# Performance work log

Hardware: AMD Instinct MI355X
Metric: run time of the kernel (lower is better)

Reference implementation:

```python
import jax, jax.numpy as jnp
import numpy as np

B, N, K, D, H = 16384, 10, 5, 512, 2
HD = D // H  # 256
IMG = 512.0


def setup_inputs() -> dict:
    key = jax.random.key(0)
    ks = jax.random.split(key, 18)
    w = lambda k, shape: (jax.random.normal(k, shape) * 0.02).astype(jnp.float32)
    boxes = jax.random.uniform(ks[0], (B, N, 4), minval=0.0, maxval=IMG, dtype=jnp.float32)
    return {
        'boxes': boxes,
        'w_in': w(ks[1], (D, K * 4)), 'b_in': jnp.zeros((D,), jnp.float32),
        'wqkv': w(ks[2], (3 * D, D)), 'bqkv': jnp.zeros((3 * D,), jnp.float32),
        'wo': w(ks[3], (D, D)), 'bo': jnp.zeros((D,), jnp.float32),
        'ln1_w': jnp.ones((D,), jnp.float32), 'ln1_b': jnp.zeros((D,), jnp.float32),
        'w1': w(ks[4], (D, D)), 'b1': jnp.zeros((D,), jnp.float32),
        'w2': w(ks[5], (D, D)), 'b2': jnp.zeros((D,), jnp.float32),
        'ln2_w': jnp.ones((D,), jnp.float32), 'ln2_b': jnp.zeros((D,), jnp.float32),
        'lnf_w': jnp.ones((D,), jnp.float32), 'lnf_b': jnp.zeros((D,), jnp.float32),
    }


def _ln(x, w, b, eps=1e-5):
    mu = jnp.mean(x, -1, keepdims=True)
    var = jnp.mean((x - mu) ** 2, -1, keepdims=True)
    return (x - mu) * jax.lax.rsqrt(var + eps) * w + b


def _relationships(boxes):
    # boxes: [B, N, 4] -> rel: [B, N, K*4]
    cx = (boxes[..., 0] + boxes[..., 2]) * 0.5 / IMG
    cy = (boxes[..., 1] + boxes[..., 3]) * 0.5 / IMG
    bw = jnp.abs(boxes[..., 2] - boxes[..., 0]) / IMG
    bh = jnp.abs(boxes[..., 3] - boxes[..., 1]) / IMG
    feats = jnp.stack([cx, cy, bw, bh], -1)  # [B, N, 4]
    dx = cx[:, :, None] - cx[:, None, :]
    dy = cy[:, :, None] - cy[:, None, :]
    dists = dx * dx + dy * dy  # [B, N, N]
    dists = jnp.where(jnp.eye(N, dtype=bool), jnp.inf, dists)
    _, idx = jax.lax.top_k(-dists, K)  # K smallest, ascending -> [B, N, K]
    nbr = jnp.take_along_axis(jnp.broadcast_to(feats[:, None], (B, N, N, 4)), idx[:, :, :, None], axis=2)  # [B, N, K, 4]
    return (nbr - feats[:, :, None, :]).reshape(B, N, K * 4)


def reference(boxes, w_in, b_in, wqkv, bqkv, wo, bo, ln1_w, ln1_b, w1, b1, w2, b2, ln2_w, ln2_b, lnf_w, lnf_b):
    rel = _relationships(boxes)                      # [B, N, 20]
    x = rel @ w_in.T + b_in                          # [B, N, D]
    # --- self attention (post-norm TransformerEncoderLayer, eval mode: no dropout) ---
    qkv = x @ wqkv.T + bqkv
    q, k, v = jnp.split(qkv, 3, axis=-1)
    split_heads = lambda t: t.reshape(B, N, H, HD).transpose(0, 2, 1, 3)
    q, k, v = split_heads(q), split_heads(k), split_heads(v)
    scores = jnp.einsum('bhqd,bhkd->bhqk', q, k) / jnp.sqrt(jnp.float32(HD))
    att = jax.nn.softmax(scores, axis=-1)
    o = jnp.einsum('bhqk,bhkd->bhqd', att, v).transpose(0, 2, 1, 3).reshape(B, N, D)
    x = _ln(x + o @ wo.T + bo, ln1_w, ln1_b)
    # --- feed forward ---
    ff = jax.nn.gelu(x @ w1.T + b1, approximate=False) @ w2.T + b2
    x = _ln(x + ff, ln2_w, ln2_b)
    return _ln(x, lnf_w, lnf_b)
```

## Files before the change

### kernel.cpp

```cpp
#include <hip/hip_runtime.h>
#include <hip/hip_bf16.h>
#include <math.h>

#define B_   16384
#define NT   10
#define KNN  5
#define D_   512
#define MTOT (B_*NT)

typedef __bf16 bf;
typedef __bf16 bfrag8 __attribute__((ext_vector_type(8)));
typedef float  floatx4 __attribute__((ext_vector_type(4)));

__device__ __forceinline__ float tof(bf x) { return (float)x; }
__device__ __forceinline__ bf    tob(float x) { return (bf)x; }

#define GLD_LDS(g, l) __builtin_amdgcn_global_load_lds( \
    (const __attribute__((address_space(1))) void*)(g), \
    (__attribute__((address_space(3))) void*)(l), 16, 0, 0)

__global__ void prep_folds(const float* __restrict__ wqkv, const float* __restrict__ bqkv,
                           const float* __restrict__ wo,   const float* __restrict__ bo,
                           bf* __restrict__ At, bf* __restrict__ Ct,
                           float* __restrict__ wconst, float* __restrict__ uvec)
{
    int gid = blockIdx.x, tid = threadIdx.x;
    if (gid < 4096) {
        int idx = gid * 256 + tid;
        int mat = idx >> 18;
        int rem = idx & 262143;
        int row = rem >> 9, col = rem & 511;
        float acc = 0.f;
        if (mat < 2) {
            int h = mat;
            const float* wq = wqkv + (size_t)(h * 256) * 512;
            const float* wk = wqkv + (size_t)(512 + h * 256) * 512;
            for (int c = 0; c < 256; ++c)
                acc += wq[c * 512 + col] * wk[c * 512 + row];
            At[(size_t)h * 262144 + row * 512 + col] = tob(acc * 0.0625f);
        } else {
            int h = mat - 2;
            const float* wv = wqkv + (size_t)(1024 + h * 256) * 512;
            for (int e = 0; e < 256; ++e)
                acc += wv[e * 512 + col] * wo[row * 512 + h * 256 + e];
            Ct[(size_t)h * 262144 + row * 512 + col] = tob(acc);
        }
    } else {
        for (int d = tid; d < 512; d += 256) {
            float acc = bo[d];
            for (int e = 0; e < 512; ++e)
                acc += bqkv[1024 + e] * wo[d * 512 + e];
            wconst[d] = acc;
            for (int h = 0; h < 2; ++h) {
                float u = 0.f;
                for (int c = 0; c < 256; ++c)
                    u += wqkv[(size_t)(512 + h * 256 + c) * 512 + d] * bqkv[h * 256 + c];
                uvec[h * 512 + d] = u * 0.0625f;
            }
        }
    }
}

__global__ void cvt_w(const float* __restrict__ src, bf* __restrict__ dst)
{
    int i = blockIdx.x * 256 + threadIdx.x;
    float4 v = *(const float4*)(src + (size_t)i * 4);
    bf4_store: ;
    bf o[4] = { tob(v.x), tob(v.y), tob(v.z), tob(v.w) };
    *(unsigned long long*)(dst + (size_t)i * 4) = *(unsigned long long*)o;
}

__global__ void rel_kernel(const float* __restrict__ boxes, float* __restrict__ rel)
{
#pragma clang fp contract(off)
    int gid = blockIdx.x * blockDim.x + threadIdx.x;
    if (gid >= MTOT) return;
    int b = gid / NT, n = gid % NT;
    const float* bx = boxes + (size_t)b * NT * 4;
    float cx[NT], cy[NT], bw[NT], bh[NT];
#pragma unroll
    for (int j = 0; j < NT; ++j) {
        float x0 = bx[j * 4 + 0], y0 = bx[j * 4 + 1];
        float x1 = bx[j * 4 + 2], y1 = bx[j * 4 + 3];
        cx[j] = ((x0 + x1) * 0.5f) * (1.f / 512.f);
        cy[j] = ((y0 + y1) * 0.5f) * (1.f / 512.f);
        bw[j] = fabsf(x1 - x0) * (1.f / 512.f);
        bh[j] = fabsf(y1 - y0) * (1.f / 512.f);
    }
    float dist[NT];
#pragma unroll
    for (int j = 0; j < NT; ++j) {
        float dx = cx[n] - cx[j], dy = cy[n] - cy[j];
        float dxx = dx * dx, dyy = dy * dy;
        dist[j] = (j == n) ? __builtin_inff() : (dxx + dyy);
    }
    float ocx = cx[n], ocy = cy[n], obw = bw[n], obh = bh[n];
#pragma unroll
    for (int k = 0; k < KNN; ++k) {
        int best = 0; float bd = __builtin_inff();
#pragma unroll
        for (int j = 0; j < NT; ++j)
            if (dist[j] < bd) { bd = dist[j]; best = j; }
        float fx = 0, fy = 0, fw = 0, fh = 0;
#pragma unroll
        for (int j = 0; j < NT; ++j)
            if (j == best) { fx = cx[j]; fy = cy[j]; fw = bw[j]; fh = bh[j]; dist[j] = __builtin_inff(); }
        size_t o = (size_t)gid * 20 + k * 4;
        rel[o + 0] = fx - ocx;
        rel[o + 1] = fy - ocy;
        rel[o + 2] = fw - obw;
        rel[o + 3] = fh - obh;
    }
}

__global__ void gemm_in(const float* __restrict__ rel, const float* __restrict__ w_in,
                        const float* __restrict__ b_in, bf* __restrict__ x0)
{
    __shared__ float relS[128][20];
    int tid = threadIdx.x;
    size_t tok0 = (size_t)blockIdx.x * 128;
    for (int i = tid; i < 128 * 20; i += 256)
        relS[i / 20][i % 20] = rel[tok0 * 20 + i];
    float w0[20], w1r[20];
#pragma unroll
    for (int j = 0; j < 20; ++j) {
        w0[j]  = w_in[tid * 20 + j];
        w1r[j] = w_in[(tid + 256) * 20 + j];
    }
    float bias0 = b_in[tid], bias1 = b_in[tid + 256];
    __syncthreads();
    for (int tk = 0; tk < 128; ++tk) {
        float a0 = bias0, a1 = bias1;
#pragma unroll
        for (int j = 0; j < 20; ++j) {
            float r = relS[tk][j];
            a0 += r * w0[j];
            a1 += r * w1r[j];
        }
        x0[(tok0 + tk) * 512 + tid]       = tob(a0);
        x0[(tok0 + tk) * 512 + tid + 256] = tob(a1);
    }
}

template <int EPI>
__launch_bounds__(256)
__global__ void gemm512(const bf* __restrict__ A, const bf* __restrict__ Bt,
                        bf* __restrict__ out, const float* __restrict__ biasf)
{
    __shared__ bf As[128 * 64];
    __shared__ bf Bs[128 * 64];
    int tid = threadIdx.x;
    int w = tid >> 6, l = tid & 63;
    int lq = l >> 4, lr = l & 15;
    int m0 = blockIdx.y * 128;
    int n0 = blockIdx.x * 128;
    int wm = (w & 1) * 64, wn = (w >> 1) * 64;
    floatx4 acc[4][4] = {};

    for (int kt = 0; kt < 8; ++kt) {
        int kb = kt * 64;
        __syncthreads();
#pragma unroll
        for (int i = 0; i < 4; ++i) {
            int chunk = i * 256 + tid;
            int mm = chunk & 127, kc = chunk >> 7;
            GLD_LDS(A  + (size_t)(m0 + mm) * 512 + kb + kc * 8, As + (i * 256 + w * 64) * 8);
            GLD_LDS(Bt + (size_t)(n0 + mm) * 512 + kb + kc * 8, Bs + (i * 256 + w * 64) * 8);
        }
        __syncthreads();
#pragma unroll
        for (int s = 0; s < 2; ++s) {
            bfrag8 af[4], bfv[4];
#pragma unroll
            for (int i = 0; i < 4; ++i)
                af[i] = *(const bfrag8*)(As + (size_t)((s * 4 + lq) * 128 + wm + i * 16 + lr) * 8);
#pragma unroll
            for (int j = 0; j < 4; ++j)
                bfv[j] = *(const bfrag8*)(Bs + (size_t)((s * 4 + lq) * 128 + wn + j * 16 + lr) * 8);
#pragma unroll
            for (int i = 0; i < 4; ++i)
#pragma unroll
                for (int j = 0; j < 4; ++j)
                    acc[i][j] = __builtin_amdgcn_mfma_f32_16x16x32_bf16(af[i], bfv[j], acc[i][j], 0, 0, 0);
        }
    }
#pragma unroll
    for (int i = 0; i < 4; ++i)
#pragma unroll
        for (int j = 0; j < 4; ++j) {
            int col = n0 + wn + j * 16 + lr;
#pragma unroll
            for (int r = 0; r < 4; ++r) {
                int row = m0 + wm + i * 16 + lq * 4 + r;
                float v = acc[i][j][r];
                if (EPI == 1) { v += biasf[col]; v = 0.5f * v * (1.f + erff(v * 0.70710678118654752f)); }
                if (EPI == 2) v += biasf[col];
                if (EPI == 3) v += tof(out[(size_t)row * 512 + col]);
                out[(size_t)row * 512 + col] = tob(v);
            }
        }
}

__global__ void scores_kernel(const bf* __restrict__ t, const bf* __restrict__ x0,
                              const float* __restrict__ uvec_h, float* __restrict__ att)
{
    int tid = threadIdx.x;
    int w = tid >> 6, l = tid & 63;
    int lq = l >> 4, lr = l & 15;
    size_t b = (size_t)blockIdx.x * 4 + w;
    const bf* trow = t  + (b * NT + lr) * 512;
    const bf* xrow = x0 + (b * NT + lr) * 512;
    floatx4 acc = {0.f, 0.f, 0.f, 0.f};
    float xu = 0.f;
#pragma unroll
    for (int kk = 0; kk < 16; ++kk) {
        bfrag8 a  = *(const bfrag8*)(trow + kk * 32 + lq * 8);
        bfrag8 bb = *(const bfrag8*)(xrow + kk * 32 + lq * 8);
        acc = __builtin_amdgcn_mfma_f32_16x16x32_bf16(a, bb, acc, 0, 0, 0);
#pragma unroll
        for (int jj = 0; jj < 8; ++jj)
            xu += (float)bb[jj] * uvec_h[kk * 32 + lq * 8 + jj];
    }
    xu += __shfl_xor(xu, 16);
    xu += __shfl_xor(xu, 32);
    bool jvalid = (lr < NT);
    float* ab = att + b * 100;
#pragma unroll
    for (int r = 0; r < 4; ++r) {
        float v = jvalid ? (acc[r] + xu) : -__builtin_inff();
        float m = v;
        m = fmaxf(m, __shfl_xor(m, 1)); m = fmaxf(m, __shfl_xor(m, 2));
        m = fmaxf(m, __shfl_xor(m, 4)); m = fmaxf(m, __shfl_xor(m, 8));
        float e = jvalid ? __expf(v - m) : 0.f;
        float s = e;
        s += __shfl_xor(s, 1); s += __shfl_xor(s, 2);
        s += __shfl_xor(s, 4); s += __shfl_xor(s, 8);
        float a = e / s;
        int i = lq * 4 + r;
        if (jvalid && i < NT) ab[i * 10 + lr] = a;
    }
}

__global__ void zmix(const float* __restrict__ att, const bf* __restrict__ x0, bf* __restrict__ z)
{
    __shared__ float xs[NT][512];
    __shared__ float as[100];
    size_t b = blockIdx.x;
    int tid = threadIdx.x;
    const bf* xb = x0 + b * NT * 512;
    for (int i = tid; i < NT * 512; i += 256) xs[i >> 9][i & 511] = tof(xb[i]);
    for (int i = tid; i < 100; i += 256) as[i] = att[b * 100 + i];
    __syncthreads();
    bf* zb = z + b * NT * 512;
    for (int o = tid; o < NT * 512; o += 256) {
        int i = o >> 9, d = o & 511;
        float a = 0.f;
#pragma unroll
        for (int j = 0; j < NT; ++j) a += as[i * 10 + j] * xs[j][d];
        zb[o] = tob(a);
    }
}

__global__ void ln_kernel(const bf* __restrict__ xin, const bf* __restrict__ yin,
                          const float* __restrict__ w, const float* __restrict__ bias,
                          bf* __restrict__ xout)
{
    int tid = threadIdx.x;
    int wv = tid >> 6, l = tid & 63;
    size_t tok = (size_t)blockIdx.x * 4 + wv;
    bfrag8 xv = *(const bfrag8*)(xin + tok * 512 + l * 8);
    bfrag8 yv = *(const bfrag8*)(yin + tok * 512 + l * 8);
    float v[8]; float s = 0.f;
#pragma unroll
    for (int i = 0; i < 8; ++i) { v[i] = (float)xv[i] + (float)yv[i]; s += v[i]; }
#pragma unroll
    for (int m = 1; m < 64; m <<= 1) s += __shfl_xor(s, m);
    float mu = s * (1.f / 512.f);
    float vs = 0.f;
#pragma unroll
    for (int i = 0; i < 8; ++i) { float d = v[i] - mu; vs += d * d; }
#pragma unroll
    for (int m = 1; m < 64; m <<= 1) vs += __shfl_xor(vs, m);
    float r = rsqrtf(vs * (1.f / 512.f) + 1e-5f);
    bfrag8 ov;
#pragma unroll
    for (int i = 0; i < 8; ++i) {
        int d = l * 8 + i;
        ov[i] = tob((v[i] - mu) * r * w[d] + bias[d]);
    }
    *(bfrag8*)(xout + tok * 512 + l * 8) = ov;
}

__global__ void final_kernel(const bf* __restrict__ x1, const bf* __restrict__ ff2,
                             const float* __restrict__ w2, const float* __restrict__ b2,
                             const float* __restrict__ wf, const float* __restrict__ bfi,
                             float* __restrict__ out)
{
    int tid = threadIdx.x;
    int wv = tid >> 6, l = tid & 63;
    size_t tok = (size_t)blockIdx.x * 4 + wv;
    bfrag8 xv = *(const bfrag8*)(x1 + tok * 512 + l * 8);
    bfrag8 yv = *(const bfrag8*)(ff2 + tok * 512 + l * 8);
    float v[8]; float s = 0.f;
#pragma unroll
    for (int i = 0; i < 8; ++i) { v[i] = (float)xv[i] + (float)yv[i]; s += v[i]; }
#pragma unroll
    for (int m = 1; m < 64; m <<= 1) s += __shfl_xor(s, m);
    float mu = s * (1.f / 512.f);
    float vs = 0.f;
#pragma unroll
    for (int i = 0; i < 8; ++i) { float d = v[i] - mu; vs += d * d; }
#pragma unroll
    for (int m = 1; m < 64; m <<= 1) vs += __shfl_xor(vs, m);
    float r = rsqrtf(vs * (1.f / 512.f) + 1e-5f);
    float u[8]; float s2 = 0.f;
#pragma unroll
    for (int i = 0; i < 8; ++i) {
        int d = l * 8 + i;
        u[i] = (v[i] - mu) * r * w2[d] + b2[d];
        s2 += u[i];
    }
#pragma unroll
    for (int m = 1; m < 64; m <<= 1) s2 += __shfl_xor(s2, m);
    float mu2 = s2 * (1.f / 512.f);
    float vs2 = 0.f;
#pragma unroll
    for (int i = 0; i < 8; ++i) { float d = u[i] - mu2; vs2 += d * d; }
#pragma unroll
    for (int m = 1; m < 64; m <<= 1) vs2 += __shfl_xor(vs2, m);
    float r2 = rsqrtf(vs2 * (1.f / 512.f) + 1e-5f);
    float4 o0, o1;
    float* op = (float*)&o0;
#pragma unroll
    for (int i = 0; i < 4; ++i) op[i] = (u[i] - mu2) * r2 * wf[l * 8 + i] + bfi[l * 8 + i];
    op = (float*)&o1;
#pragma unroll
    for (int i = 0; i < 4; ++i) op[i] = (u[4 + i] - mu2) * r2 * wf[l * 8 + 4 + i] + bfi[l * 8 + 4 + i];
    *(float4*)(out + tok * 512 + l * 8) = o0;
    *(float4*)(out + tok * 512 + l * 8 + 4) = o1;
}

extern "C" void kernel_launch(void* const* d_in, const int* in_sizes, int n_in,
                              void* d_out, int out_size, void* d_ws, size_t ws_size,
                              hipStream_t stream)
{
    const float* boxes = (const float*)d_in[0];
    const float* w_in  = (const float*)d_in[1];
    const float* b_in  = (const float*)d_in[2];
    const float* wqkv  = (const float*)d_in[3];
    const float* bqkv  = (const float*)d_in[4];
    const float* wo    = (const float*)d_in[5];
    const float* bo    = (const float*)d_in[6];
    const float* ln1w  = (const float*)d_in[7];
    const float* ln1b  = (const float*)d_in[8];
    const float* w1    = (const float*)d_in[9];
    const float* b1    = (const float*)d_in[10];
    const float* w2    = (const float*)d_in[11];
    const float* b2    = (const float*)d_in[12];
    const float* ln2w  = (const float*)d_in[13];
    const float* ln2b  = (const float*)d_in[14];
    const float* lnfw  = (const float*)d_in[15];
    const float* lnfb  = (const float*)d_in[16];
    float* out = (float*)d_out;

    char* ws = (char*)d_ws;
    bf*    At     = (bf*)(ws + 0);
    bf*    Ct     = (bf*)(ws + 1048576);
    bf*    W1b    = (bf*)(ws + 2097152);
    bf*    W2b    = (bf*)(ws + 2621440);
    float* wconst = (float*)(ws + 3145728);
    float* uvec   = (float*)(ws + 3147776);
    float* att    = (float*)(ws + 3151872);
    bf*    x0     = (bf*)(ws + 16259072);
    bf*    t      = (bf*)(ws + 184047616);
    bf*    y      = (bf*)(ws + 351836160);
    float* rel    = (float*)(ws + 184047616);

    dim3 gblk(256);
    dim3 ggemm(4, MTOT / 128);

    prep_folds<<<4097, gblk, 0, stream>>>(wqkv, bqkv, wo, bo, At, Ct, wconst, uvec);
    cvt_w<<<256, gblk, 0, stream>>>(w1, W1b);
    cvt_w<<<256, gblk, 0, stream>>>(w2, W2b);
    rel_kernel<<<(MTOT + 255) / 256, gblk, 0, stream>>>(boxes, rel);
    gemm_in<<<MTOT / 128, gblk, 0, stream>>>(rel, w_in, b_in, x0);

    gemm512<0><<<ggemm, gblk, 0, stream>>>(x0, At, t, nullptr);
    scores_kernel<<<B_ / 4, gblk, 0, stream>>>(t, x0, uvec, att);
    gemm512<0><<<ggemm, gblk, 0, stream>>>(x0, At + 262144, t, nullptr);
    scores_kernel<<<B_ / 4, gblk, 0, stream>>>(t, x0, uvec + 512, att + (size_t)B_ * 100);
    zmix<<<B_, gblk, 0, stream>>>(att, x0, t);
    gemm512<2><<<ggemm, gblk, 0, stream>>>(t, Ct, y, wconst);
    zmix<<<B_, gblk, 0, stream>>>(att + (size_t)B_ * 100, x0, t);
    gemm512<3><<<ggemm, gblk, 0, stream>>>(t, Ct + 262144, y, nullptr);
    ln_kernel<<<MTOT / 4, gblk, 0, stream>>>(x0, y, ln1w, ln1b, x0);
    gemm512<1><<<ggemm, gblk, 0, stream>>>(x0, W1b, t, b1);
    gemm512<2><<<ggemm, gblk, 0, stream>>>(t, W2b, y, b2);
    final_kernel<<<MTOT / 4, gblk, 0, stream>>>(x0, y, ln2w, ln2b, lnfw, lnfb, out);
}
```

Before: 2.578 ms.

## Fuse whole encoder layer into one persistent per-tile kernel with LDS-resident activations

Replaces the chain of separate kernels (input projection, per-head folded QK GEMMs, scores, zmix, output GEMMs, layernorms, FFN GEMMs, final LN) with a single kernel. Each block processes 80 tokens (8 batches of 10), keeping activations in swizzled LDS buffers and streaming weight fragments directly from global memory into MFMA operands with register double-buffering. This removes the large global round-trips of intermediate activations and the many kernel launches. In exchange, each block rereads every weight matrix, and the large LDS footprint and register use limit occupancy.

```diff
diff --git a/kernel.cpp b/kernel.cpp
--- a/kernel.cpp
+++ b/kernel.cpp
@@ -15,9 +15,12 @@
 __device__ __forceinline__ float tof(bf x) { return (float)x; }
 __device__ __forceinline__ bf    tob(float x) { return (bf)x; }
 
-#define GLD_LDS(g, l) __builtin_amdgcn_global_load_lds( \
-    (const __attribute__((address_space(1))) void*)(g), \
-    (__attribute__((address_space(3))) void*)(l), 16, 0, 0)
+__device__ __forceinline__ void sw_st16(bf* lds, int row, int col, bf v) {
+    *(bf*)((char*)lds + row * 1024 + ((col * 2) ^ ((row & 7) << 4))) = v;
+}
+__device__ __forceinline__ bf sw_ld16(const bf* lds, int row, int col) {
+    return *(const bf*)((const char*)lds + row * 1024 + ((col * 2) ^ ((row & 7) << 4)));
+}
 
 __global__ void prep_folds(const float* __restrict__ wqkv, const float* __restrict__ bqkv,
                            const float* __restrict__ wo,   const float* __restrict__ bo,
@@ -65,7 +68,6 @@
 {
     int i = blockIdx.x * 256 + threadIdx.x;
     float4 v = *(const float4*)(src + (size_t)i * 4);
-    bf4_store: ;
     bf o[4] = { tob(v.x), tob(v.y), tob(v.z), tob(v.w) };
     *(unsigned long long*)(dst + (size_t)i * 4) = *(unsigned long long*)o;
 }
@@ -113,231 +115,362 @@
     }
 }
 
-__global__ void gemm_in(const float* __restrict__ rel, const float* __restrict__ w_in,
-                        const float* __restrict__ b_in, bf* __restrict__ x0)
-{
-    __shared__ float relS[128][20];
-    int tid = threadIdx.x;
-    size_t tok0 = (size_t)blockIdx.x * 128;
-    for (int i = tid; i < 128 * 20; i += 256)
-        relS[i / 20][i % 20] = rel[tok0 * 20 + i];
-    float w0[20], w1r[20];
-#pragma unroll
-    for (int j = 0; j < 20; ++j) {
-        w0[j]  = w_in[tid * 20 + j];
-        w1r[j] = w_in[(tid + 256) * 20 + j];
-    }
-    float bias0 = b_in[tid], bias1 = b_in[tid + 256];
-    __syncthreads();
-    for (int tk = 0; tk < 128; ++tk) {
-        float a0 = bias0, a1 = bias1;
-#pragma unroll
-        for (int j = 0; j < 20; ++j) {
-            float r = relS[tk][j];
-            a0 += r * w0[j];
-            a1 += r * w1r[j];
-        }
-        x0[(tok0 + tk) * 512 + tid]       = tob(a0);
-        x0[(tok0 + tk) * 512 + tid + 256] = tob(a1);
-    }
-}
-
-template <int EPI>
-__launch_bounds__(256)
-__global__ void gemm512(const bf* __restrict__ A, const bf* __restrict__ Bt,
-                        bf* __restrict__ out, const float* __restrict__ biasf)
-{
-    __shared__ bf As[128 * 64];
-    __shared__ bf Bs[128 * 64];
-    int tid = threadIdx.x;
-    int w = tid >> 6, l = tid & 63;
-    int lq = l >> 4, lr = l & 15;
-    int m0 = blockIdx.y * 128;
-    int n0 = blockIdx.x * 128;
-    int wm = (w & 1) * 64, wn = (w >> 1) * 64;
-    floatx4 acc[4][4] = {};
-
-    for (int kt = 0; kt < 8; ++kt) {
-        int kb = kt * 64;
-        __syncthreads();
-#pragma unroll
-        for (int i = 0; i < 4; ++i) {
-            int chunk = i * 256 + tid;
-            int mm = chunk & 127, kc = chunk >> 7;
-            GLD_LDS(A  + (size_t)(m0 + mm) * 512 + kb + kc * 8, As + (i * 256 + w * 64) * 8);
-            GLD_LDS(Bt + (size_t)(n0 + mm) * 512 + kb + kc * 8, Bs + (i * 256 + w * 64) * 8);
-        }
-        __syncthreads();
-#pragma unroll
-        for (int s = 0; s < 2; ++s) {
-            bfrag8 af[4], bfv[4];
-#pragma unroll
-            for (int i = 0; i < 4; ++i)
-                af[i] = *(const bfrag8*)(As + (size_t)((s * 4 + lq) * 128 + wm + i * 16 + lr) * 8);
+__device__ __forceinline__ void gemm_ph(const bf* INlds, const bf* __restrict__ W,
+                                        floatx4 (&acc)[5][4], int w, int lq, int lr,
+                                        const int (&rb0)[5], const int (&sw0)[5])
+{
+    const bf* Wb = W + (size_t)(w * 64 + lr) * 512 + lq * 8;
+    bfrag8 bv[4], bn[4];
+#pragma unroll
+    for (int j = 0; j < 4; ++j) bv[j] = *(const bfrag8*)(Wb + (size_t)j * 8192);
+    for (int ks = 0; ks < 16; ++ks) {
+        if (ks < 15) {
 #pragma unroll
             for (int j = 0; j < 4; ++j)
-                bfv[j] = *(const bfrag8*)(Bs + (size_t)((s * 4 + lq) * 128 + wn + j * 16 + lr) * 8);
-#pragma unroll
-            for (int i = 0; i < 4; ++i)
-#pragma unroll
-                for (int j = 0; j < 4; ++j)
-                    acc[i][j] = __builtin_amdgcn_mfma_f32_16x16x32_bf16(af[i], bfv[j], acc[i][j], 0, 0, 0);
-        }
-    }
-#pragma unroll
-    for (int i = 0; i < 4; ++i)
-#pragma unroll
-        for (int j = 0; j < 4; ++j) {
-            int col = n0 + wn + j * 16 + lr;
-#pragma unroll
-            for (int r = 0; r < 4; ++r) {
-                int row = m0 + wm + i * 16 + lq * 4 + r;
-                float v = acc[i][j][r];
-                if (EPI == 1) { v += biasf[col]; v = 0.5f * v * (1.f + erff(v * 0.70710678118654752f)); }
-                if (EPI == 2) v += biasf[col];
-                if (EPI == 3) v += tof(out[(size_t)row * 512 + col]);
-                out[(size_t)row * 512 + col] = tob(v);
-            }
-        }
-}
-
-__global__ void scores_kernel(const bf* __restrict__ t, const bf* __restrict__ x0,
-                              const float* __restrict__ uvec_h, float* __restrict__ att)
-{
-    int tid = threadIdx.x;
-    int w = tid >> 6, l = tid & 63;
-    int lq = l >> 4, lr = l & 15;
-    size_t b = (size_t)blockIdx.x * 4 + w;
-    const bf* trow = t  + (b * NT + lr) * 512;
-    const bf* xrow = x0 + (b * NT + lr) * 512;
-    floatx4 acc = {0.f, 0.f, 0.f, 0.f};
+                bn[j] = *(const bfrag8*)(Wb + (size_t)j * 8192 + (ks + 1) * 32);
+        }
+        int cb = ks * 64 + lq * 16;
+        bfrag8 af[5];
+#pragma unroll
+        for (int i = 0; i < 5; ++i)
+            af[i] = *(const bfrag8*)((const char*)INlds + (rb0[i] + (cb ^ sw0[i])));
+#pragma unroll
+        for (int i = 0; i < 5; ++i)
+#pragma unroll
+            for (int j = 0; j < 4; ++j)
+                acc[i][j] = __builtin_amdgcn_mfma_f32_16x16x32_bf16(af[i], bv[j], acc[i][j], 0, 0, 0);
+#pragma unroll
+        for (int j = 0; j < 4; ++j) bv[j] = bn[j];
+    }
+}
+
+__device__ __forceinline__ void scores_z(const bf* Xs, bf* Ts, const float* __restrict__ uvec_h,
+                                         int w, int l, int lq, int lr)
+{
+    int rb = w * 10;
+    int arow = rb + (lr < 10 ? lr : 0);
+    int abase = arow * 1024, asw = (arow & 7) << 4;
+    floatx4 sacc = {0.f, 0.f, 0.f, 0.f};
     float xu = 0.f;
 #pragma unroll
     for (int kk = 0; kk < 16; ++kk) {
-        bfrag8 a  = *(const bfrag8*)(trow + kk * 32 + lq * 8);
-        bfrag8 bb = *(const bfrag8*)(xrow + kk * 32 + lq * 8);
-        acc = __builtin_amdgcn_mfma_f32_16x16x32_bf16(a, bb, acc, 0, 0, 0);
+        int cb = kk * 64 + lq * 16;
+        bfrag8 a  = *(const bfrag8*)((const char*)Ts + abase + (cb ^ asw));
+        bfrag8 bb = *(const bfrag8*)((const char*)Xs + abase + (cb ^ asw));
+        sacc = __builtin_amdgcn_mfma_f32_16x16x32_bf16(a, bb, sacc, 0, 0, 0);
 #pragma unroll
         for (int jj = 0; jj < 8; ++jj)
             xu += (float)bb[jj] * uvec_h[kk * 32 + lq * 8 + jj];
     }
     xu += __shfl_xor(xu, 16);
     xu += __shfl_xor(xu, 32);
-    bool jvalid = (lr < NT);
-    float* ab = att + b * 100;
+    bool jv = (lr < 10);
+    float a_r[4];
 #pragma unroll
     for (int r = 0; r < 4; ++r) {
-        float v = jvalid ? (acc[r] + xu) : -__builtin_inff();
+        float v = jv ? (sacc[r] + xu) : -__builtin_inff();
         float m = v;
         m = fmaxf(m, __shfl_xor(m, 1)); m = fmaxf(m, __shfl_xor(m, 2));
         m = fmaxf(m, __shfl_xor(m, 4)); m = fmaxf(m, __shfl_xor(m, 8));
-        float e = jvalid ? __expf(v - m) : 0.f;
+        float e = jv ? __expf(v - m) : 0.f;
         float s = e;
         s += __shfl_xor(s, 1); s += __shfl_xor(s, 2);
         s += __shfl_xor(s, 4); s += __shfl_xor(s, 8);
-        float a = e / s;
-        int i = lq * 4 + r;
-        if (jvalid && i < NT) ab[i * 10 + lr] = a;
-    }
-}
-
-__global__ void zmix(const float* __restrict__ att, const bf* __restrict__ x0, bf* __restrict__ z)
-{
-    __shared__ float xs[NT][512];
-    __shared__ float as[100];
-    size_t b = blockIdx.x;
+        a_r[r] = e / s;
+    }
+    bfrag8 xj[10];
+#pragma unroll
+    for (int j = 0; j < 10; ++j) {
+        int row = rb + j;
+        xj[j] = *(const bfrag8*)((const char*)Xs + row * 1024 + ((l * 16) ^ ((row & 7) << 4)));
+    }
+#pragma unroll
+    for (int i = 0; i < 10; ++i) {
+        float zz[8] = {0, 0, 0, 0, 0, 0, 0, 0};
+#pragma unroll
+        for (int j = 0; j < 10; ++j) {
+            float aij = __shfl(a_r[i & 3], ((i >> 2) << 4) + j);
+#pragma unroll
+            for (int q = 0; q < 8; ++q) zz[q] += aij * (float)xj[j][q];
+        }
+        bfrag8 zv;
+#pragma unroll
+        for (int q = 0; q < 8; ++q) zv[q] = tob(zz[q]);
+        int row = rb + i;
+        *(bfrag8*)((char*)Ts + row * 1024 + ((l * 16) ^ ((row & 7) << 4))) = zv;
+    }
+}
+
+__global__ __launch_bounds__(512, 2)
+void fused(const float* __restrict__ rel, const float* __restrict__ w_in,
+           const float* __restrict__ b_in,
+           const bf* __restrict__ At, const bf* __restrict__ Ct,
+           const float* __restrict__ uvec, const float* __restrict__ wconst,
+           const bf* __restrict__ W1b, const float* __restrict__ b1,
+           const bf* __restrict__ W2b, const float* __restrict__ b2,
+           const float* __restrict__ l1w, const float* __restrict__ l1b,
+           const float* __restrict__ l2w, const float* __restrict__ l2b,
+           const float* __restrict__ lfw, const float* __restrict__ lfb,
+           float* __restrict__ out)
+{
+    __shared__ __align__(16) bf Xs[40960];
+    __shared__ __align__(16) bf Ts[40960];
     int tid = threadIdx.x;
-    const bf* xb = x0 + b * NT * 512;
-    for (int i = tid; i < NT * 512; i += 256) xs[i >> 9][i & 511] = tof(xb[i]);
-    for (int i = tid; i < 100; i += 256) as[i] = att[b * 100 + i];
+    int w = tid >> 6, l = tid & 63, lq = l >> 4, lr = l & 15;
+    size_t tok0 = (size_t)blockIdx.x * 80;
+
+    {
+        float* relS = (float*)Ts;
+        for (int i = tid; i < 1600; i += 512) relS[i] = rel[tok0 * 20 + i];
+    }
     __syncthreads();
-    bf* zb = z + b * NT * 512;
-    for (int o = tid; o < NT * 512; o += 256) {
-        int i = o >> 9, d = o & 511;
-        float a = 0.f;
-#pragma unroll
-        for (int j = 0; j < NT; ++j) a += as[i * 10 + j] * xs[j][d];
-        zb[o] = tob(a);
-    }
-}
-
-__global__ void ln_kernel(const bf* __restrict__ xin, const bf* __restrict__ yin,
-                          const float* __restrict__ w, const float* __restrict__ bias,
-                          bf* __restrict__ xout)
-{
-    int tid = threadIdx.x;
-    int wv = tid >> 6, l = tid & 63;
-    size_t tok = (size_t)blockIdx.x * 4 + wv;
-    bfrag8 xv = *(const bfrag8*)(xin + tok * 512 + l * 8);
-    bfrag8 yv = *(const bfrag8*)(yin + tok * 512 + l * 8);
-    float v[8]; float s = 0.f;
-#pragma unroll
-    for (int i = 0; i < 8; ++i) { v[i] = (float)xv[i] + (float)yv[i]; s += v[i]; }
-#pragma unroll
-    for (int m = 1; m < 64; m <<= 1) s += __shfl_xor(s, m);
-    float mu = s * (1.f / 512.f);
-    float vs = 0.f;
-#pragma unroll
-    for (int i = 0; i < 8; ++i) { float d = v[i] - mu; vs += d * d; }
-#pragma unroll
-    for (int m = 1; m < 64; m <<= 1) vs += __shfl_xor(vs, m);
-    float r = rsqrtf(vs * (1.f / 512.f) + 1e-5f);
-    bfrag8 ov;
-#pragma unroll
-    for (int i = 0; i < 8; ++i) {
-        int d = l * 8 + i;
-        ov[i] = tob((v[i] - mu) * r * w[d] + bias[d]);
-    }
-    *(bfrag8*)(xout + tok * 512 + l * 8) = ov;
-}
-
-__global__ void final_kernel(const bf* __restrict__ x1, const bf* __restrict__ ff2,
-                             const float* __restrict__ w2, const float* __restrict__ b2,
-                             const float* __restrict__ wf, const float* __restrict__ bfi,
-                             float* __restrict__ out)
-{
-    int tid = threadIdx.x;
-    int wv = tid >> 6, l = tid & 63;
-    size_t tok = (size_t)blockIdx.x * 4 + wv;
-    bfrag8 xv = *(const bfrag8*)(x1 + tok * 512 + l * 8);
-    bfrag8 yv = *(const bfrag8*)(ff2 + tok * 512 + l * 8);
-    float v[8]; float s = 0.f;
-#pragma unroll
-    for (int i = 0; i < 8; ++i) { v[i] = (float)xv[i] + (float)yv[i]; s += v[i]; }
-#pragma unroll
-    for (int m = 1; m < 64; m <<= 1) s += __shfl_xor(s, m);
-    float mu = s * (1.f / 512.f);
-    float vs = 0.f;
-#pragma unroll
-    for (int i = 0; i < 8; ++i) { float d = v[i] - mu; vs += d * d; }
-#pragma unroll
-    for (int m = 1; m < 64; m <<= 1) vs += __shfl_xor(vs, m);
-    float r = rsqrtf(vs * (1.f / 512.f) + 1e-5f);
-    float u[8]; float s2 = 0.f;
-#pragma unroll
-    for (int i = 0; i < 8; ++i) {
-        int d = l * 8 + i;
-        u[i] = (v[i] - mu) * r * w2[d] + b2[d];
-        s2 += u[i];
-    }
-#pragma unroll
-    for (int m = 1; m < 64; m <<= 1) s2 += __shfl_xor(s2, m);
-    float mu2 = s2 * (1.f / 512.f);
-    float vs2 = 0.f;
-#pragma unroll
-    for (int i = 0; i < 8; ++i) { float d = u[i] - mu2; vs2 += d * d; }
-#pragma unroll
-    for (int m = 1; m < 64; m <<= 1) vs2 += __shfl_xor(vs2, m);
-    float r2 = rsqrtf(vs2 * (1.f / 512.f) + 1e-5f);
-    float4 o0, o1;
-    float* op = (float*)&o0;
-#pragma unroll
-    for (int i = 0; i < 4; ++i) op[i] = (u[i] - mu2) * r2 * wf[l * 8 + i] + bfi[l * 8 + i];
-    op = (float*)&o1;
-#pragma unroll
-    for (int i = 0; i < 4; ++i) op[i] = (u[4 + i] - mu2) * r2 * wf[l * 8 + 4 + i] + bfi[l * 8 + 4 + i];
-    *(float4*)(out + tok * 512 + l * 8) = o0;
-    *(float4*)(out + tok * 512 + l * 8 + 4) = o1;
+    {
+        const float* relS = (const float*)Ts;
+        float wreg[20];
+#pragma unroll
+        for (int k = 0; k < 20; ++k) wreg[k] = w_in[tid * 20 + k];
+        float bias = b_in[tid];
+        for (int r = 0; r < 80; ++r) {
+            float a = bias;
+#pragma unroll
+            for (int k = 0; k < 20; ++k) a += relS[r * 20 + k] * wreg[k];
+            sw_st16(Xs, r, tid, tob(a));
+        }
+    }
+    __syncthreads();
+
+    floatx4 acc[5][4];
+    floatx4 accY[5][4];
+    float   mus[5][4];
+    int rb0[5], sw0[5];
+#pragma unroll
+    for (int i = 0; i < 5; ++i) { int row = i * 16 + lr; rb0[i] = row * 1024; sw0[i] = (row & 7) << 4; }
+
+    for (int h = 0; h < 2; ++h) {
+#pragma unroll
+        for (int i = 0; i < 5; ++i)
+#pragma unroll
+            for (int j = 0; j < 4; ++j) acc[i][j] = (floatx4){0.f, 0.f, 0.f, 0.f};
+        gemm_ph(Xs, At + (size_t)h * 262144, acc, w, lq, lr, rb0, sw0);
+#pragma unroll
+        for (int i = 0; i < 5; ++i)
+#pragma unroll
+            for (int j = 0; j < 4; ++j) {
+                int col = w * 64 + j * 16 + lr;
+#pragma unroll
+                for (int r = 0; r < 4; ++r)
+                    sw_st16(Ts, i * 16 + lq * 4 + r, col, tob(acc[i][j][r]));
+            }
+        __syncthreads();
+        scores_z(Xs, Ts, uvec + h * 512, w, l, lq, lr);
+        __syncthreads();
+        if (h == 0) {
+#pragma unroll
+            for (int j = 0; j < 4; ++j) {
+                float wc = wconst[w * 64 + j * 16 + lr];
+#pragma unroll
+                for (int i = 0; i < 5; ++i) accY[i][j] = (floatx4){wc, wc, wc, wc};
+            }
+        }
+        gemm_ph(Ts, Ct + (size_t)h * 262144, accY, w, lq, lr, rb0, sw0);
+        __syncthreads();
+    }
+
+    {
+        float* scr  = (float*)Ts;
+        float* scr2 = scr + 640;
+        float lnw[4], lnb[4];
+#pragma unroll
+        for (int j = 0; j < 4; ++j) { lnw[j] = l1w[w * 64 + j * 16 + lr]; lnb[j] = l1b[w * 64 + j * 16 + lr]; }
+#pragma unroll
+        for (int i = 0; i < 5; ++i)
+#pragma unroll
+            for (int r = 0; r < 4; ++r) {
+                int row = i * 16 + lq * 4 + r;
+                float ps = 0.f;
+#pragma unroll
+                for (int j = 0; j < 4; ++j) {
+                    int col = w * 64 + j * 16 + lr;
+                    float v = accY[i][j][r] + tof(sw_ld16(Xs, row, col));
+                    accY[i][j][r] = v;
+                    ps += v;
+                }
+                ps += __shfl_xor(ps, 1); ps += __shfl_xor(ps, 2);
+                ps += __shfl_xor(ps, 4); ps += __shfl_xor(ps, 8);
+                if (lr == 0) scr[row * 8 + w] = ps;
+            }
+        __syncthreads();
+#pragma unroll
+        for (int i = 0; i < 5; ++i)
+#pragma unroll
+            for (int r = 0; r < 4; ++r) {
+                int row = i * 16 + lq * 4 + r;
+                float s = 0.f;
+#pragma unroll
+                for (int q = 0; q < 8; ++q) s += scr[row * 8 + q];
+                float mu = s * (1.f / 512.f);
+                mus[i][r] = mu;
+                float ps2 = 0.f;
+#pragma unroll
+                for (int j = 0; j < 4; ++j) { float d = accY[i][j][r] - mu; ps2 += d * d; }
+                ps2 += __shfl_xor(ps2, 1); ps2 += __shfl_xor(ps2, 2);
+                ps2 += __shfl_xor(ps2, 4); ps2 += __shfl_xor(ps2, 8);
+                if (lr == 0) scr2[row * 8 + w] = ps2;
+            }
+        __syncthreads();
+#pragma unroll
+        for (int i = 0; i < 5; ++i)
+#pragma unroll
+            for (int r = 0; r < 4; ++r) {
+                int row = i * 16 + lq * 4 + r;
+                float s2 = 0.f;
+#pragma unroll
+                for (int q = 0; q < 8; ++q) s2 += scr2[row * 8 + q];
+                float rstd = rsqrtf(s2 * (1.f / 512.f) + 1e-5f);
+#pragma unroll
+                for (int j = 0; j < 4; ++j) {
+                    int col = w * 64 + j * 16 + lr;
+                    sw_st16(Xs, row, col, tob((accY[i][j][r] - mus[i][r]) * rstd * lnw[j] + lnb[j]));
+                }
+            }
+        __syncthreads();
+    }
+
+    {
+#pragma unroll
+        for (int i = 0; i < 5; ++i)
+#pragma unroll
+            for (int j = 0; j < 4; ++j) acc[i][j] = (floatx4){0.f, 0.f, 0.f, 0.f};
+        gemm_ph(Xs, W1b, acc, w, lq, lr, rb0, sw0);
+        float b1c[4];
+#pragma unroll
+        for (int j = 0; j < 4; ++j) b1c[j] = b1[w * 64 + j * 16 + lr];
+#pragma unroll
+        for (int i = 0; i < 5; ++i)
+#pragma unroll
+            for (int j = 0; j < 4; ++j) {
+                int col = w * 64 + j * 16 + lr;
+#pragma unroll
+                for (int r = 0; r < 4; ++r) {
+                    float v = acc[i][j][r] + b1c[j];
+                    v = 0.5f * v * (1.f + erff(v * 0.70710678118654752f));
+                    sw_st16(Ts, i * 16 + lq * 4 + r, col, tob(v));
+                }
+            }
+        __syncthreads();
+    }
+
+    {
+#pragma unroll
+        for (int i = 0; i < 5; ++i)
+#pragma unroll
+            for (int j = 0; j < 4; ++j) acc[i][j] = (floatx4){0.f, 0.f, 0.f, 0.f};
+        gemm_ph(Ts, W2b, acc, w, lq, lr, rb0, sw0);
+        __syncthreads();
+    }
+
+    {
+        float* scr  = (float*)Ts;
+        float* scr2 = scr + 640;
+        float b2c[4], w2c[4], bb2[4], wfc[4], bfc[4];
+#pragma unroll
+        for (int j = 0; j < 4; ++j) {
+            int col = w * 64 + j * 16 + lr;
+            b2c[j] = b2[col]; w2c[j] = l2w[col]; bb2[j] = l2b[col];
+            wfc[j] = lfw[col]; bfc[j] = lfb[col];
+        }
+#pragma unroll
+        for (int i = 0; i < 5; ++i)
+#pragma unroll
+            for (int r = 0; r < 4; ++r) {
+                int row = i * 16 + lq * 4 + r;
+                float ps = 0.f;
+#pragma unroll
+                for (int j = 0; j < 4; ++j) {
+                    int col = w * 64 + j * 16 + lr;
+                    float v = acc[i][j][r] + tof(sw_ld16(Xs, row, col)) + b2c[j];
+                    acc[i][j][r] = v;
+                    ps += v;
+                }
+                ps += __shfl_xor(ps, 1); ps += __shfl_xor(ps, 2);
+                ps += __shfl_xor(ps, 4); ps += __shfl_xor(ps, 8);
+                if (lr == 0) scr[row * 8 + w] = ps;
+            }
+        __syncthreads();
+#pragma unroll
+        for (int i = 0; i < 5; ++i)
+#pragma unroll
+            for (int r = 0; r < 4; ++r) {
+                int row = i * 16 + lq * 4 + r;
+                float s = 0.f;
+#pragma unroll
+                for (int q = 0; q < 8; ++q) s += scr[row * 8 + q];
+                float mu = s * (1.f / 512.f);
+                mus[i][r] = mu;
+                float ps2 = 0.f;
+#pragma unroll
+                for (int j = 0; j < 4; ++j) { float d = acc[i][j][r] - mu; ps2 += d * d; }
+                ps2 += __shfl_xor(ps2, 1); ps2 += __shfl_xor(ps2, 2);
+                ps2 += __shfl_xor(ps2, 4); ps2 += __shfl_xor(ps2, 8);
+                if (lr == 0) scr2[row * 8 + w] = ps2;
+            }
+        __syncthreads();
+#pragma unroll
+        for (int i = 0; i < 5; ++i)
+#pragma unroll
+            for (int r = 0; r < 4; ++r) {
+                int row = i * 16 + lq * 4 + r;
+                float s2 = 0.f;
+#pragma unroll
+                for (int q = 0; q < 8; ++q) s2 += scr2[row * 8 + q];
+                float rstd = rsqrtf(s2 * (1.f / 512.f) + 1e-5f);
+                float ps = 0.f;
+#pragma unroll
+                for (int j = 0; j < 4; ++j) {
+                    float u = (acc[i][j][r] - mus[i][r]) * rstd * w2c[j] + bb2[j];
+                    acc[i][j][r] = u;
+                    ps += u;
+                }
+                ps += __shfl_xor(ps, 1); ps += __shfl_xor(ps, 2);
+                ps += __shfl_xor(ps, 4); ps += __shfl_xor(ps, 8);
+                if (lr == 0) scr[row * 8 + w] = ps;
+            }
+        __syncthreads();
+#pragma unroll
+        for (int i = 0; i < 5; ++i)
+#pragma unroll
+            for (int r = 0; r < 4; ++r) {
+                int row = i * 16 + lq * 4 + r;
+                float s = 0.f;
+#pragma unroll
+                for (int q = 0; q < 8; ++q) s += scr[row * 8 + q];
+                float mu = s * (1.f / 512.f);
+                mus[i][r] = mu;
+                float ps2 = 0.f;
+#pragma unroll
+                for (int j = 0; j < 4; ++j) { float d = acc[i][j][r] - mu; ps2 += d * d; }
+                ps2 += __shfl_xor(ps2, 1); ps2 += __shfl_xor(ps2, 2);
+                ps2 += __shfl_xor(ps2, 4); ps2 += __shfl_xor(ps2, 8);
+                if (lr == 0) scr2[row * 8 + w] = ps2;
+            }
+        __syncthreads();
+#pragma unroll
+        for (int i = 0; i < 5; ++i)
+#pragma unroll
+            for (int r = 0; r < 4; ++r) {
+                int row = i * 16 + lq * 4 + r;
+                float s2 = 0.f;
+#pragma unroll
+                for (int q = 0; q < 8; ++q) s2 += scr2[row * 8 + q];
+                float rstd = rsqrtf(s2 * (1.f / 512.f) + 1e-5f);
+#pragma unroll
+                for (int j = 0; j < 4; ++j) {
+                    int col = w * 64 + j * 16 + lr;
+                    out[(tok0 + row) * 512 + col] =
+                        (acc[i][j][r] - mus[i][r]) * rstd * wfc[j] + bfc[j];
+                }
+            }
+    }
 }
 
 extern "C" void kernel_launch(void* const* d_in, const int* in_sizes, int n_in,
@@ -370,31 +503,16 @@
     bf*    W2b    = (bf*)(ws + 2621440);
     float* wconst = (float*)(ws + 3145728);
     float* uvec   = (float*)(ws + 3147776);
-    float* att    = (float*)(ws + 3151872);
-    bf*    x0     = (bf*)(ws + 16259072);
-    bf*    t      = (bf*)(ws + 184047616);
-    bf*    y      = (bf*)(ws + 351836160);
-    float* rel    = (float*)(ws + 184047616);
+    float* rel    = (float*)(ws + 3151872);
 
     dim3 gblk(256);
-    dim3 ggemm(4, MTOT / 128);
 
     prep_folds<<<4097, gblk, 0, stream>>>(wqkv, bqkv, wo, bo, At, Ct, wconst, uvec);
     cvt_w<<<256, gblk, 0, stream>>>(w1, W1b);
     cvt_w<<<256, gblk, 0, stream>>>(w2, W2b);
     rel_kernel<<<(MTOT + 255) / 256, gblk, 0, stream>>>(boxes, rel);
-    gemm_in<<<MTOT / 128, gblk, 0, stream>>>(rel, w_in, b_in, x0);
-
-    gemm512<0><<<ggemm, gblk, 0, stream>>>(x0, At, t, nullptr);
-    scores_kernel<<<B_ / 4, gblk, 0, stream>>>(t, x0, uvec, att);
-    gemm512<0><<<ggemm, gblk, 0, stream>>>(x0, At + 262144, t, nullptr);
-    scores_kernel<<<B_ / 4, gblk, 0, stream>>>(t, x0, uvec + 512, att + (size_t)B_ * 100);
-    zmix<<<B_, gblk, 0, stream>>>(att, x0, t);
-    gemm512<2><<<ggemm, gblk, 0, stream>>>(t, Ct, y, wconst);
-    zmix<<<B_, gblk, 0, stream>>>(att + (size_t)B_ * 100, x0, t);
-    gemm512<3><<<ggemm, gblk, 0, stream>>>(t, Ct + 262144, y, nullptr);
-    ln_kernel<<<MTOT / 4, gblk, 0, stream>>>(x0, y, ln1w, ln1b, x0);
-    gemm512<1><<<ggemm, gblk, 0, stream>>>(x0, W1b, t, b1);
-    gemm512<2><<<ggemm, gblk, 0, stream>>>(t, W2b, y, b2);
-    final_kernel<<<MTOT / 4, gblk, 0, stream>>>(x0, y, ln2w, ln2b, lnfw, lnfb, out);
-}
+
+    fused<<<MTOT / 80, 512, 0, stream>>>(rel, w_in, b_in, At, Ct, uvec, wconst,
+                                         W1b, b1, W2b, b2,
+                                         ln1w, ln1b, ln2w, ln2b, lnfw, lnfb, out);
+}
```

After: 2.624 ms. No clear change (+1.8%).
